# Optimization experiments

Measured on AMD Instinct MI355X. Metric: run time of the kernel, lower is better.

Reference implementation:

```python
import jax, jax.numpy as jnp
import numpy as np

B, E, H, V, L, N = 16, 512, 512, 32000, 512, 20  # batch, embed, hidden, vocab, max_code_len, max_node_num


def setup_inputs() -> dict:
    key = jax.random.key(0)
    ks = jax.random.split(key, 20)
    s = 0.02
    f32 = jnp.float32
    return {
        "y": jax.random.randint(ks[0], (B,), 0, V),
        "q": jax.random.normal(ks[1], (B, N, L, 2 * H), f32),
        "q_n": jax.random.normal(ks[2], (B, N, 2 * H), f32),
        "g": jax.random.normal(ks[3], (B, N, 2 * H), f32),
        "embed": jax.random.normal(ks[4], (V, E), f32) * s,
        "fc_w": jax.random.normal(ks[5], (H, 4 * H), f32) * s,
        "fc_b": jnp.zeros((H,), f32),
        "w_ih": jax.random.normal(ks[6], (3 * H, E), f32) * s,
        "w_hh": jax.random.normal(ks[7], (3 * H, H), f32) * s,
        "b_ih": jnp.zeros((3 * H,), f32),
        "b_hh": jnp.zeros((3 * H,), f32),
        "w_ga": jax.random.normal(ks[8], (H, 2 * H), f32) * s,
        "w_la": jax.random.normal(ks[9], (H, 2 * H), f32) * s,
        "wv_w": jax.random.normal(ks[10], (L, 5 * H), f32) * s,
        "wv_b": jnp.zeros((L,), f32),
        "wh_w": jax.random.normal(ks[11], (1, H), f32) * s,
        "wc_w": jax.random.normal(ks[12], (1, 2 * H), f32) * s,
        "wy_w": jax.random.normal(ks[13], (1, E), f32) * s,
        "fco_w": jax.random.normal(ks[14], (V, L), f32) * s,
        "fco_b": jnp.zeros((V,), f32),
    }


def reference(y, q, q_n, g, embed, fc_w, fc_b, w_ih, w_hh, b_ih, b_hh,
              w_ga, w_la, wv_w, wv_b, wh_w, wc_w, wy_w, fco_w, fco_b):
    # --- slice the first node / first position (as in the torch code) ---
    g_t = g[:, 0, :]        # [B, 2H]
    qn_t = q_n[:, 0, :]     # [B, 2H]
    q_t = q[:, 0, :, :]     # [B, L, 2H]

    com_embed = embed[y][:, None, :]                        # [B, 1, E]
    h0 = jnp.concatenate([qn_t, g_t], axis=1) @ fc_w.T + fc_b  # [B, H]

    # --- single GRU step (PyTorch GRU cell math) ---
    x = com_embed[:, 0, :]
    gi = x @ w_ih.T + b_ih                                  # [B, 3H]
    gh = h0 @ w_hh.T + b_hh                                 # [B, 3H]
    r = jax.nn.sigmoid(gi[:, :H] + gh[:, :H])
    z = jax.nn.sigmoid(gi[:, H:2 * H] + gh[:, H:2 * H])
    n = jnp.tanh(gi[:, 2 * H:] + r * gh[:, 2 * H:])
    h = (1.0 - z) * n + z * h0
    out = h[:, None, :]                                     # [B, 1, H]

    # --- graph attention over nodes ---
    g_proj = jnp.einsum('bnd,hd->bnh', g, w_ga)             # [B, N, H]
    gamma = jax.nn.softmax(jnp.einsum('bth,bnh->btn', out, g_proj), axis=-1)
    cg = jnp.einsum('btn,bnd->btd', gamma, g)               # [B, 1, 2H]

    # --- local attention over code tokens ---
    q_proj = jnp.einsum('bld,hd->blh', q_t, w_la)           # [B, L, H]
    beta = jax.nn.softmax(jnp.einsum('bth,blh->btl', out, q_proj), axis=-1)
    c = jnp.einsum('btl,bld->btd', beta, q_t)               # [B, 1, 2H]

    # --- pointer-generator mixing ---
    concat = jnp.concatenate([out, c, cg], axis=2)          # [B, 1, 5H]
    P_vocab = jax.nn.softmax(concat @ wv_w.T + wv_b, axis=1)  # softmax over singleton dim (faithful)
    p_gen = jax.nn.leaky_relu(out @ wh_w.T + c @ wc_w.T + com_embed @ wy_w.T,
                              negative_slope=0.2)[:, :, 0]  # [B, 1]
    P_w = P_vocab * p_gen[:, :, None] + beta * (1.0 - p_gen)[:, :, None]
    pre = (P_w @ fco_w.T + fco_b)[:, 0, :]                  # [B, V]
    return pre
```

## Files before the change

kernel.cpp:

```cpp
#include <hip/hip_runtime.h>
#include <math.h>

#define BB 16
#define EE 512
#define HH 512
#define VV 32000
#define LL 512
#define NQ 20
#define H2 1024
#define H3 1536
#define H4 2048

#define H0_OFF   0
#define GI_OFF   8192
#define GH_OFF   32768
#define H_OFF    57344
#define UQ_OFF   65536
#define WHD_OFF  81920
#define ED_OFF   81936
#define SC_OFF   81952
#define QC_OFF   90144
#define PW_OFF   98336

__device__ __forceinline__ float wave_reduce_add(float v) {
#pragma unroll
  for (int off = 32; off > 0; off >>= 1) v += __shfl_xor(v, off, 64);
  return v;
}

__global__ __launch_bounds__(256) void k_h0_gi(
    const int* __restrict__ y, const float* __restrict__ qn, const float* __restrict__ g,
    const float* __restrict__ embed, const float* __restrict__ fc_w, const float* __restrict__ fc_b,
    const float* __restrict__ w_ih, const float* __restrict__ b_ih,
    float* __restrict__ h0_ws, float* __restrict__ gi_ws) {
  int gw = (blockIdx.x * 256 + threadIdx.x) >> 6;
  int lane = threadIdx.x & 63;
  if (gw < BB * HH) {
    int b = gw >> 9, j = gw & (HH - 1);
    const float4* fw  = (const float4*)(fc_w + (size_t)j * H4);
    const float4* qn4 = (const float4*)(qn + (size_t)b * (NQ * H2));
    const float4* g4  = (const float4*)(g  + (size_t)b * (NQ * H2));
    float acc = 0.f;
#pragma unroll
    for (int it = 0; it < 8; ++it) {
      int i4 = it * 64 + lane;
      float4 a = (i4 < 256) ? qn4[i4] : g4[i4 - 256];
      float4 w4 = fw[i4];
      acc += a.x * w4.x + a.y * w4.y + a.z * w4.z + a.w * w4.w;
    }
    acc = wave_reduce_add(acc);
    if (lane == 0) h0_ws[gw] = acc + fc_b[j];
  } else {
    int w2 = gw - BB * HH;
    int b = w2 / H3, j = w2 - b * H3;
    const float4* xr = (const float4*)(embed + (size_t)y[b] * EE);
    const float4* wr = (const float4*)(w_ih + (size_t)j * EE);
    float acc = 0.f;
#pragma unroll
    for (int it = 0; it < 2; ++it) {
      int i4 = it * 64 + lane;
      float4 a = xr[i4], w4 = wr[i4];
      acc += a.x * w4.x + a.y * w4.y + a.z * w4.z + a.w * w4.w;
    }
    acc = wave_reduce_add(acc);
    if (lane == 0) gi_ws[w2] = acc + b_ih[j];
  }
}

__global__ __launch_bounds__(256) void k_gh(
    const float* __restrict__ h0_ws, const float* __restrict__ w_hh,
    const float* __restrict__ b_hh, float* __restrict__ gh_ws) {
  int gw = (blockIdx.x * 256 + threadIdx.x) >> 6;
  int lane = threadIdx.x & 63;
  int b = gw / H3, j = gw - b * H3;
  const float4* hr = (const float4*)(h0_ws + b * HH);
  const float4* wr = (const float4*)(w_hh + (size_t)j * HH);
  float acc = 0.f;
#pragma unroll
  for (int it = 0; it < 2; ++it) {
    int i4 = it * 64 + lane;
    float4 a = hr[i4], w4 = wr[i4];
    acc += a.x * w4.x + a.y * w4.y + a.z * w4.z + a.w * w4.w;
  }
  acc = wave_reduce_add(acc);
  if (lane == 0) gh_ws[gw] = acc + b_hh[j];
}

__global__ __launch_bounds__(512) void k_gru(
    const int* __restrict__ y, const float* __restrict__ embed,
    const float* __restrict__ gi_ws, const float* __restrict__ gh_ws,
    const float* __restrict__ h0_ws,
    const float* __restrict__ wh_w, const float* __restrict__ wy_w,
    float* __restrict__ h_ws, float* __restrict__ whd_ws, float* __restrict__ ed_ws) {
  int b = blockIdx.x, j = threadIdx.x;
  const float* gi = gi_ws + b * H3;
  const float* gh = gh_ws + b * H3;
  float r = 1.f / (1.f + expf(-(gi[j] + gh[j])));
  float z = 1.f / (1.f + expf(-(gi[HH + j] + gh[HH + j])));
  float n = tanhf(gi[2 * HH + j] + r * gh[2 * HH + j]);
  float h0v = h0_ws[b * HH + j];
  float hv = (1.f - z) * n + z * h0v;
  h_ws[b * HH + j] = hv;
  float p1 = hv * wh_w[j];
  float p2 = embed[(size_t)y[b] * EE + j] * wy_w[j];
  p1 = wave_reduce_add(p1);
  p2 = wave_reduce_add(p2);
  __shared__ float red1[8], red2[8];
  int wid = j >> 6, lane = j & 63;
  if (lane == 0) { red1[wid] = p1; red2[wid] = p2; }
  __syncthreads();
  if (j == 0) {
    float s1 = 0.f, s2 = 0.f;
#pragma unroll
    for (int i = 0; i < 8; ++i) { s1 += red1[i]; s2 += red2[i]; }
    whd_ws[b] = s1;
    ed_ws[b] = s2;
  }
}

__global__ __launch_bounds__(256) void k_uq(
    const float* __restrict__ h_ws, const float* __restrict__ w_la,
    float* __restrict__ uq_ws) {
  int idx = blockIdx.x * 256 + threadIdx.x;
  int b = idx >> 10, d = idx & (H2 - 1);
  const float* hr = h_ws + b * HH;
  float acc = 0.f;
#pragma unroll 4
  for (int k = 0; k < HH; ++k) acc += hr[k] * w_la[k * H2 + d];
  uq_ws[idx] = acc;
}

__global__ __launch_bounds__(256) void k_score(
    const float* __restrict__ q, const float* __restrict__ uq_ws,
    const float* __restrict__ wc_w,
    float* __restrict__ score_ws, float* __restrict__ qc_ws) {
  int gw = (blockIdx.x * 256 + threadIdx.x) >> 6;
  int lane = threadIdx.x & 63;
  int b = gw >> 9, l = gw & (LL - 1);
  const float4* qr = (const float4*)(q + (size_t)b * NQ * LL * H2 + (size_t)l * H2);
  const float4* ur = (const float4*)(uq_ws + b * H2);
  const float4* wr = (const float4*)wc_w;
  float a1 = 0.f, a2 = 0.f;
#pragma unroll
  for (int it = 0; it < 4; ++it) {
    int i4 = it * 64 + lane;
    float4 qv = qr[i4], uv = ur[i4], wv = wr[i4];
    a1 += qv.x * uv.x + qv.y * uv.y + qv.z * uv.z + qv.w * uv.w;
    a2 += qv.x * wv.x + qv.y * wv.y + qv.z * wv.z + qv.w * wv.w;
  }
  a1 = wave_reduce_add(a1);
  a2 = wave_reduce_add(a2);
  if (lane == 0) { score_ws[gw] = a1; qc_ws[gw] = a2; }
}

__global__ __launch_bounds__(512) void k_softmax(
    const float* __restrict__ score_ws, const float* __restrict__ qc_ws,
    const float* __restrict__ whd_ws, const float* __restrict__ ed_ws,
    float* __restrict__ pw_ws) {
  int b = blockIdx.x, l = threadIdx.x;
  float s = score_ws[b * LL + l];
  float qc = qc_ws[b * LL + l];
  __shared__ float redm[8], red_e[8], red_q[8];
  int wid = l >> 6, lane = l & 63;
  float m = s;
#pragma unroll
  for (int off = 32; off > 0; off >>= 1) m = fmaxf(m, __shfl_xor(m, off, 64));
  if (lane == 0) redm[wid] = m;
  __syncthreads();
  float mm = redm[0];
#pragma unroll
  for (int i = 1; i < 8; ++i) mm = fmaxf(mm, redm[i]);
  float e = expf(s - mm);
  float se = wave_reduce_add(e);
  float sq = wave_reduce_add(e * qc);
  if (lane == 0) { red_e[wid] = se; red_q[wid] = sq; }
  __syncthreads();
  float Se = 0.f, Sq = 0.f;
#pragma unroll
  for (int i = 0; i < 8; ++i) { Se += red_e[i]; Sq += red_q[i]; }
  float inv = 1.f / Se;
  float c_dot = Sq * inv;
  float p = whd_ws[b] + c_dot + ed_ws[b];
  float pg = p > 0.f ? p : 0.2f * p;
  pw_ws[b * LL + l] = pg + (e * inv) * (1.f - pg);
}

__global__ __launch_bounds__(256) void k_final(
    const float* __restrict__ pw_ws, const float* __restrict__ fco_w,
    const float* __restrict__ fco_b, float* __restrict__ out) {
  __shared__ float plds[16 * 516];
  int tid = threadIdx.x;
#pragma unroll
  for (int it = 0; it < 8; ++it) {
    int i4 = it * 256 + tid;
    int row = i4 >> 7;
    int col = (i4 & 127) * 4;
    float4 v = ((const float4*)pw_ws)[i4];
    *(float4*)&plds[row * 516 + col] = v;
  }
  __syncthreads();
  int v = blockIdx.x * 16 + (tid & 15);
  int b = tid >> 4;
  const float4* fr = (const float4*)(fco_w + (size_t)v * LL);
  const float4* pr = (const float4*)&plds[b * 516];
  float acc = 0.f;
#pragma unroll 8
  for (int k4 = 0; k4 < 128; ++k4) {
    float4 f = fr[k4];
    float4 p = pr[k4];
    acc += f.x * p.x + f.y * p.y + f.z * p.z + f.w * p.w;
  }
  out[(size_t)b * VV + v] = acc + fco_b[v];
}

extern "C" void kernel_launch(void* const* d_in, const int* in_sizes, int n_in,
                              void* d_out, int out_size, void* d_ws, size_t ws_size,
                              hipStream_t stream) {
  const int*   y     = (const int*)d_in[0];
  const float* q     = (const float*)d_in[1];
  const float* qn    = (const float*)d_in[2];
  const float* g     = (const float*)d_in[3];
  const float* embed = (const float*)d_in[4];
  const float* fc_w  = (const float*)d_in[5];
  const float* fc_b  = (const float*)d_in[6];
  const float* w_ih  = (const float*)d_in[7];
  const float* w_hh  = (const float*)d_in[8];
  const float* b_ih  = (const float*)d_in[9];
  const float* b_hh  = (const float*)d_in[10];
  const float* w_la  = (const float*)d_in[12];
  const float* wh_w  = (const float*)d_in[15];
  const float* wc_w  = (const float*)d_in[16];
  const float* wy_w  = (const float*)d_in[17];
  const float* fco_w = (const float*)d_in[18];
  const float* fco_b = (const float*)d_in[19];
  float* ws  = (float*)d_ws;
  float* out = (float*)d_out;

  k_h0_gi<<<8192, 256, 0, stream>>>(y, qn, g, embed, fc_w, fc_b, w_ih, b_ih,
                                    ws + H0_OFF, ws + GI_OFF);
  k_gh<<<6144, 256, 0, stream>>>(ws + H0_OFF, w_hh, b_hh, ws + GH_OFF);
  k_gru<<<BB, 512, 0, stream>>>(y, embed, ws + GI_OFF, ws + GH_OFF, ws + H0_OFF,
                                wh_w, wy_w, ws + H_OFF, ws + WHD_OFF, ws + ED_OFF);
  k_uq<<<64, 256, 0, stream>>>(ws + H_OFF, w_la, ws + UQ_OFF);
  k_score<<<2048, 256, 0, stream>>>(q, ws + UQ_OFF, wc_w, ws + SC_OFF, ws + QC_OFF);
  k_softmax<<<BB, 512, 0, stream>>>(ws + SC_OFF, ws + QC_OFF, ws + WHD_OFF,
                                    ws + ED_OFF, ws + PW_OFF);
  k_final<<<2000, 256, 0, stream>>>(ws + PW_OFF, fco_w, fco_b, out);
}
```

Before: 191.8 us.

## Reuse weight rows across batch in GEMV kernels and split-K the uq projection

The h0/gi and gh kernels now assign one wavefront per output row and keep that row's weights in registers while looping over all 16 batch entries. Before, each (batch, row) pair reloaded the same weight row, so weight traffic is cut by the batch factor and far fewer blocks are launched. k_uq now splits K across 4 waves with a shared-memory reduction and launches 256 blocks instead of 64, giving more parallelism. The cost is higher register use (16 accumulators plus the cached weights) and 16 serialized wave reductions per wavefront.

```diff
diff --git a/kernel.cpp b/kernel.cpp
--- a/kernel.cpp
+++ b/kernel.cpp
@@ -28,42 +28,56 @@
   return v;
 }
 
-__global__ __launch_bounds__(256) void k_h0_gi(
+__global__ __launch_bounds__(256) void k_in_gemm(
     const int* __restrict__ y, const float* __restrict__ qn, const float* __restrict__ g,
-    const float* __restrict__ embed, const float* __restrict__ fc_w, const float* __restrict__ fc_b,
+    const float* __restrict__ embed,
+    const float* __restrict__ fc_w, const float* __restrict__ fc_b,
     const float* __restrict__ w_ih, const float* __restrict__ b_ih,
     float* __restrict__ h0_ws, float* __restrict__ gi_ws) {
   int gw = (blockIdx.x * 256 + threadIdx.x) >> 6;
   int lane = threadIdx.x & 63;
-  if (gw < BB * HH) {
-    int b = gw >> 9, j = gw & (HH - 1);
-    const float4* fw  = (const float4*)(fc_w + (size_t)j * H4);
-    const float4* qn4 = (const float4*)(qn + (size_t)b * (NQ * H2));
-    const float4* g4  = (const float4*)(g  + (size_t)b * (NQ * H2));
-    float acc = 0.f;
-#pragma unroll
-    for (int it = 0; it < 8; ++it) {
-      int i4 = it * 64 + lane;
-      float4 a = (i4 < 256) ? qn4[i4] : g4[i4 - 256];
-      float4 w4 = fw[i4];
-      acc += a.x * w4.x + a.y * w4.y + a.z * w4.z + a.w * w4.w;
-    }
-    acc = wave_reduce_add(acc);
-    if (lane == 0) h0_ws[gw] = acc + fc_b[j];
+  if (gw < HH) {
+    int j = gw;
+    const float4* fw = (const float4*)(fc_w + (size_t)j * H4);
+    float4 w[8];
+#pragma unroll
+    for (int it = 0; it < 8; ++it) w[it] = fw[it * 64 + lane];
+    float acc[16];
+#pragma unroll
+    for (int b = 0; b < 16; ++b) {
+      const float4* qn4 = (const float4*)(qn + (size_t)b * (NQ * H2));
+      const float4* g4  = (const float4*)(g  + (size_t)b * (NQ * H2));
+      float a = 0.f;
+#pragma unroll
+      for (int it = 0; it < 8; ++it) {
+        int i4 = it * 64 + lane;
+        float4 av = (i4 < 256) ? qn4[i4] : g4[i4 - 256];
+        a += av.x * w[it].x + av.y * w[it].y + av.z * w[it].z + av.w * w[it].w;
+      }
+      acc[b] = a;
+    }
+#pragma unroll
+    for (int b = 0; b < 16; ++b) {
+      float s = wave_reduce_add(acc[b]);
+      if (lane == b) h0_ws[b * HH + j] = s + fc_b[j];
+    }
   } else {
-    int w2 = gw - BB * HH;
-    int b = w2 / H3, j = w2 - b * H3;
-    const float4* xr = (const float4*)(embed + (size_t)y[b] * EE);
+    int j = gw - HH;
     const float4* wr = (const float4*)(w_ih + (size_t)j * EE);
-    float acc = 0.f;
-#pragma unroll
-    for (int it = 0; it < 2; ++it) {
-      int i4 = it * 64 + lane;
-      float4 a = xr[i4], w4 = wr[i4];
-      acc += a.x * w4.x + a.y * w4.y + a.z * w4.z + a.w * w4.w;
-    }
-    acc = wave_reduce_add(acc);
-    if (lane == 0) gi_ws[w2] = acc + b_ih[j];
+    float4 w0 = wr[lane], w1 = wr[64 + lane];
+    float acc[16];
+#pragma unroll
+    for (int b = 0; b < 16; ++b) {
+      const float4* xr = (const float4*)(embed + (size_t)y[b] * EE);
+      float4 a0 = xr[lane], a1 = xr[64 + lane];
+      acc[b] = a0.x * w0.x + a0.y * w0.y + a0.z * w0.z + a0.w * w0.w
+             + a1.x * w1.x + a1.y * w1.y + a1.z * w1.z + a1.w * w1.w;
+    }
+#pragma unroll
+    for (int b = 0; b < 16; ++b) {
+      float s = wave_reduce_add(acc[b]);
+      if (lane == b) gi_ws[b * H3 + j] = s + b_ih[j];
+    }
   }
 }
 
@@ -72,18 +86,22 @@
     const float* __restrict__ b_hh, float* __restrict__ gh_ws) {
   int gw = (blockIdx.x * 256 + threadIdx.x) >> 6;
   int lane = threadIdx.x & 63;
-  int b = gw / H3, j = gw - b * H3;
-  const float4* hr = (const float4*)(h0_ws + b * HH);
+  int j = gw;
   const float4* wr = (const float4*)(w_hh + (size_t)j * HH);
-  float acc = 0.f;
-#pragma unroll
-  for (int it = 0; it < 2; ++it) {
-    int i4 = it * 64 + lane;
-    float4 a = hr[i4], w4 = wr[i4];
-    acc += a.x * w4.x + a.y * w4.y + a.z * w4.z + a.w * w4.w;
-  }
-  acc = wave_reduce_add(acc);
-  if (lane == 0) gh_ws[gw] = acc + b_hh[j];
+  float4 w0 = wr[lane], w1 = wr[64 + lane];
+  float acc[16];
+#pragma unroll
+  for (int b = 0; b < 16; ++b) {
+    const float4* hr = (const float4*)(h0_ws + b * HH);
+    float4 a0 = hr[lane], a1 = hr[64 + lane];
+    acc[b] = a0.x * w0.x + a0.y * w0.y + a0.z * w0.z + a0.w * w0.w
+           + a1.x * w1.x + a1.y * w1.y + a1.z * w1.z + a1.w * w1.w;
+  }
+#pragma unroll
+  for (int b = 0; b < 16; ++b) {
+    float s = wave_reduce_add(acc[b]);
+    if (lane == b) gh_ws[b * H3 + j] = s + b_hh[j];
+  }
 }
 
 __global__ __launch_bounds__(512) void k_gru(
@@ -101,10 +119,8 @@
   float h0v = h0_ws[b * HH + j];
   float hv = (1.f - z) * n + z * h0v;
   h_ws[b * HH + j] = hv;
-  float p1 = hv * wh_w[j];
-  float p2 = embed[(size_t)y[b] * EE + j] * wy_w[j];
-  p1 = wave_reduce_add(p1);
-  p2 = wave_reduce_add(p2);
+  float p1 = wave_reduce_add(hv * wh_w[j]);
+  float p2 = wave_reduce_add(embed[(size_t)y[b] * EE + j] * wy_w[j]);
   __shared__ float red1[8], red2[8];
   int wid = j >> 6, lane = j & 63;
   if (lane == 0) { red1[wid] = p1; red2[wid] = p2; }
@@ -121,13 +137,23 @@
 __global__ __launch_bounds__(256) void k_uq(
     const float* __restrict__ h_ws, const float* __restrict__ w_la,
     float* __restrict__ uq_ws) {
-  int idx = blockIdx.x * 256 + threadIdx.x;
-  int b = idx >> 10, d = idx & (H2 - 1);
-  const float* hr = h_ws + b * HH;
+  int b = blockIdx.x >> 4;
+  int dt = blockIdx.x & 15;
+  int dl = threadIdx.x & 63;
+  int ks = threadIdx.x >> 6;
+  const float* hr = h_ws + b * HH + ks * 128;
+  const float* wp = w_la + (size_t)(ks * 128) * H2 + dt * 64 + dl;
   float acc = 0.f;
-#pragma unroll 4
-  for (int k = 0; k < HH; ++k) acc += hr[k] * w_la[k * H2 + d];
-  uq_ws[idx] = acc;
+#pragma unroll 8
+  for (int k = 0; k < 128; ++k) acc += hr[k] * wp[(size_t)k * H2];
+  __shared__ float red[4][64];
+  red[ks][dl] = acc;
+  __syncthreads();
+  if (threadIdx.x < 64) {
+    float s = red[0][threadIdx.x] + red[1][threadIdx.x]
+            + red[2][threadIdx.x] + red[3][threadIdx.x];
+    uq_ws[b * H2 + dt * 64 + threadIdx.x] = s;
+  }
 }
 
 __global__ __launch_bounds__(256) void k_score(
@@ -236,12 +262,12 @@
   float* ws  = (float*)d_ws;
   float* out = (float*)d_out;
 
-  k_h0_gi<<<8192, 256, 0, stream>>>(y, qn, g, embed, fc_w, fc_b, w_ih, b_ih,
-                                    ws + H0_OFF, ws + GI_OFF);
-  k_gh<<<6144, 256, 0, stream>>>(ws + H0_OFF, w_hh, b_hh, ws + GH_OFF);
+  k_in_gemm<<<512, 256, 0, stream>>>(y, qn, g, embed, fc_w, fc_b, w_ih, b_ih,
+                                     ws + H0_OFF, ws + GI_OFF);
+  k_gh<<<384, 256, 0, stream>>>(ws + H0_OFF, w_hh, b_hh, ws + GH_OFF);
   k_gru<<<BB, 512, 0, stream>>>(y, embed, ws + GI_OFF, ws + GH_OFF, ws + H0_OFF,
                                 wh_w, wy_w, ws + H_OFF, ws + WHD_OFF, ws + ED_OFF);
-  k_uq<<<64, 256, 0, stream>>>(ws + H_OFF, w_la, ws + UQ_OFF);
+  k_uq<<<256, 256, 0, stream>>>(ws + H_OFF, w_la, ws + UQ_OFF);
   k_score<<<2048, 256, 0, stream>>>(q, ws + UQ_OFF, wc_w, ws + SC_OFF, ws + QC_OFF);
   k_softmax<<<BB, 512, 0, stream>>>(ws + SC_OFF, ws + QC_OFF, ws + WHD_OFF,
                                     ws + ED_OFF, ws + PW_OFF);
```

New measurement: 165.4 us. 1.16x faster.
